# Optimization experiments

Hardware: AMD Instinct MI355X
Metric: run time of the kernel (lower is better)

## Reference

```python
import jax, jax.numpy as jnp
import numpy as np

N_NODES = 50000
N_EDGES = 1600000
IN_DIM = 128
HID = [128, 128]
OUT_DIM = 64
N_USERS = 10000


def setup_inputs() -> dict:
    key = jax.random.key(0)
    ks = jax.random.split(key, 12)
    features = jax.random.normal(ks[0], (N_NODES, IN_DIM), jnp.float32)
    src = jax.random.randint(ks[1], (N_EDGES,), 0, N_NODES)
    dst = jax.random.randint(ks[2], (N_EDGES,), 0, N_NODES)
    users = jax.random.randint(ks[3], (N_USERS,), 0, N_NODES)
    s = 0.05
    W0 = jax.random.normal(ks[4], (IN_DIM, HID[0]), jnp.float32) * s
    b0 = jnp.zeros((HID[0],), jnp.float32)
    W1 = jax.random.normal(ks[5], (HID[0], HID[1]), jnp.float32) * s
    b1 = jnp.zeros((HID[1],), jnp.float32)
    Ws1 = jax.random.normal(ks[6], (HID[1], 64), jnp.float32) * s
    bs1 = jnp.zeros((64,), jnp.float32)
    Ws2 = jax.random.normal(ks[7], (64, OUT_DIM), jnp.float32) * s
    bs2 = jnp.zeros((OUT_DIM,), jnp.float32)
    return {"features": features, "W0": W0, "b0": b0, "W1": W1, "b1": b1,
            "Ws1": Ws1, "bs1": bs1, "Ws2": Ws2, "bs2": bs2,
            "src": src, "dst": dst, "users": users}


def _gcn_layer(h, src, dst, cs, cd, W, b):
    # DGL GraphConv, norm='both': relu(D_in^-1/2 A D_out^-1/2 (h W) + b)
    h = h @ W                                   # [N, d_out]
    m = (h * cs)[src]                           # [E, d_out] gathered messages
    agg = jax.ops.segment_sum(m, dst, num_segments=N_NODES)
    return jax.nn.relu(agg * cd + b)


def reference(features, W0, b0, W1, b1, Ws1, bs1, Ws2, bs2, src, dst, users):
    ones = jnp.ones(src.shape[0], jnp.float32)
    deg_out = jax.ops.segment_sum(ones, src, num_segments=N_NODES)
    deg_in = jax.ops.segment_sum(ones, dst, num_segments=N_NODES)
    cs = jnp.maximum(deg_out, 1.0)[:, None] ** -0.5  # source-side norm
    cd = jnp.maximum(deg_in, 1.0)[:, None] ** -0.5   # dest-side norm
    h = _gcn_layer(features, src, dst, cs, cd, W0, b0)
    # dropout between layers: identity in eval mode
    h = _gcn_layer(h, src, dst, cs, cd, W1, b1)
    user_h = h[users]                            # [U, HID[-1]]
    R = jnp.tanh(user_h @ Ws1 + bs1) @ Ws2 + bs2  # SR head
    return (R, h)
```

## Files before the change

### kernel.cpp

```cpp
#include <hip/hip_runtime.h>
#include <hip/hip_bf16.h>
#include <hip/hip_fp16.h>

#define NN 50000
#define NE 1600000
#define DIM 128
#define NU 10000
#define NB 256
#define SLICE_W 12500
#define NE4 (NE / 4)
#define CHUNK4 ((NE4 + NB - 1) / NB)
#define NSC 49

__global__ __launch_bounds__(512) void k_hist(const int4* __restrict__ src4,
                                              const int4* __restrict__ dst4,
                                              unsigned int* __restrict__ histD,
                                              unsigned int* __restrict__ histS) {
    __shared__ unsigned int lh[SLICE_W];
    for (int i = threadIdx.x; i < SLICE_W; i += 512) lh[i] = 0u;
    __syncthreads();
    int b = blockIdx.x & (NB - 1);
    const int4* idx4 = (blockIdx.x < NB) ? dst4 : src4;
    unsigned int* out = ((blockIdx.x < NB) ? histD : histS) + (size_t)b * SLICE_W;
    int beg = b * CHUNK4, end = min(beg + CHUNK4, NE4);
    for (int i = beg + threadIdx.x; i < end; i += 512) {
        int4 v = idx4[i];
        atomicAdd(&lh[v.x >> 2], 1u << ((v.x & 3) * 8));
        atomicAdd(&lh[v.y >> 2], 1u << ((v.y & 3) * 8));
        atomicAdd(&lh[v.z >> 2], 1u << ((v.z & 3) * 8));
        atomicAdd(&lh[v.w >> 2], 1u << ((v.w & 3) * 8));
    }
    __syncthreads();
    for (int i = threadIdx.x; i < SLICE_W; i += 512) out[i] = lh[i];
}

__global__ __launch_bounds__(256) void k_reduce_norms(const unsigned int* __restrict__ histD,
                                                      const unsigned int* __restrict__ histS,
                                                      int* __restrict__ din,
                                                      float* __restrict__ cs, float* __restrict__ cd,
                                                      int* __restrict__ partials) {
    __shared__ int red[256];
    int wi = blockIdx.x * blockDim.x + threadIdx.x;
    unsigned int d0 = 0, d1 = 0, d2 = 0, d3 = 0, s0 = 0, s1 = 0, s2 = 0, s3 = 0;
    if (wi < SLICE_W) {
        for (int b = 0; b < NB; ++b) {
            unsigned int wd = histD[(size_t)b * SLICE_W + wi];
            unsigned int ws = histS[(size_t)b * SLICE_W + wi];
            d0 += wd & 0xFFu; d1 += (wd >> 8) & 0xFFu; d2 += (wd >> 16) & 0xFFu; d3 += wd >> 24;
            s0 += ws & 0xFFu; s1 += (ws >> 8) & 0xFFu; s2 += (ws >> 16) & 0xFFu; s3 += ws >> 24;
        }
        int n = wi * 4;
        *(int4*)&din[n] = make_int4(d0, d1, d2, d3);
        float4 vcd, vcs;
        vcd.x = rsqrtf(fmaxf((float)d0, 1.f)); vcd.y = rsqrtf(fmaxf((float)d1, 1.f));
        vcd.z = rsqrtf(fmaxf((float)d2, 1.f)); vcd.w = rsqrtf(fmaxf((float)d3, 1.f));
        vcs.x = rsqrtf(fmaxf((float)s0, 1.f)); vcs.y = rsqrtf(fmaxf((float)s1, 1.f));
        vcs.z = rsqrtf(fmaxf((float)s2, 1.f)); vcs.w = rsqrtf(fmaxf((float)s3, 1.f));
        *(float4*)&cd[n] = vcd;
        *(float4*)&cs[n] = vcs;
    }
    red[threadIdx.x] = (int)(d0 + d1 + d2 + d3);
    __syncthreads();
    for (int off = 128; off > 0; off >>= 1) {
        if (threadIdx.x < off) red[threadIdx.x] += red[threadIdx.x + off];
        __syncthreads();
    }
    if (threadIdx.x == 0) partials[blockIdx.x] = red[0];
}

__global__ __launch_bounds__(64) void k_scan2(const int* __restrict__ partials,
                                              int* __restrict__ bases) {
    int lane = threadIdx.x;
    int v = (lane < NSC) ? partials[lane] : 0;
    int s = v;
    for (int off = 1; off < 64; off <<= 1) {
        int n = __shfl_up(s, off);
        if (lane >= off) s += n;
    }
    if (lane < NSC) bases[lane] = s - v;
}

__global__ __launch_bounds__(256) void k_scan3(const int* __restrict__ din,
                                               const int* __restrict__ bases,
                                               int* __restrict__ offs) {
    __shared__ int part[256];
    int t = threadIdx.x;
    int n0 = blockIdx.x * 1024 + t * 4;
    int4 d = make_int4(0, 0, 0, 0);
    if (n0 < NN) d = *(const int4*)&din[n0];
    int tsum = d.x + d.y + d.z + d.w;
    part[t] = tsum;
    __syncthreads();
    for (int off = 1; off < 256; off <<= 1) {
        int v = (t >= off) ? part[t - off] : 0;
        __syncthreads();
        part[t] += v;
        __syncthreads();
    }
    if (n0 < NN) {
        int o = bases[blockIdx.x] + part[t] - tsum;
        *(int4*)&offs[n0] = make_int4(o, o + d.x, o + d.x + d.y, o + d.x + d.y + d.z);
    }
}

__global__ __launch_bounds__(256) void k_blockbase(const unsigned int* __restrict__ histD,
                                                   unsigned char* __restrict__ rel8) {
    int n = blockIdx.x * blockDim.x + threadIdx.x;
    if (n >= NN) return;
    int wi = n >> 2, sh = (n & 3) * 8;
    unsigned int run = 0;
    for (int b = 0; b < NB; ++b) {
        rel8[(size_t)b * NN + n] = (unsigned char)run;
        run += (histD[(size_t)b * SLICE_W + wi] >> sh) & 0xFFu;
    }
}

__global__ __launch_bounds__(512) void k_scatter2(const int4* __restrict__ src4,
                                                  const int4* __restrict__ dst4,
                                                  const int* __restrict__ offs,
                                                  const unsigned char* __restrict__ rel8,
                                                  unsigned short* __restrict__ csc) {
    __shared__ unsigned int lc[SLICE_W];
    for (int i = threadIdx.x; i < SLICE_W; i += 512) lc[i] = 0u;
    __syncthreads();
    int b = blockIdx.x;
    const unsigned char* rel = rel8 + (size_t)b * NN;
    int beg = b * CHUNK4, end = min(beg + CHUNK4, NE4);
    for (int i = beg + threadIdx.x; i < end; i += 512) {
        int4 s = src4[i];
        int4 d = dst4[i];
#pragma unroll
        for (int j = 0; j < 4; ++j) {
            int dd = (j == 0) ? d.x : (j == 1) ? d.y : (j == 2) ? d.z : d.w;
            int ss = (j == 0) ? s.x : (j == 1) ? s.y : (j == 2) ? s.z : s.w;
            int sh = (dd & 3) * 8;
            unsigned int old = atomicAdd(&lc[dd >> 2], 1u << sh);
            int local = (old >> sh) & 0xFF;
            csc[offs[dd] + rel[dd] + local] = (unsigned short)ss;
        }
    }
}

__global__ __launch_bounds__(256) void k_matmul_cs(const float* __restrict__ X,
                                                   const float* __restrict__ W,
                                                   const float* __restrict__ cs,
                                                   __half* __restrict__ Y, int nrows) {
    __shared__ __half sW[DIM * DIM];
    __shared__ float sX[16][DIM];
    for (int i = threadIdx.x * 4; i < DIM * DIM; i += 256 * 4) {
        float4 w4 = *(const float4*)&W[i];
        *(__half2*)&sW[i]     = __float22half2_rn(make_float2(w4.x, w4.y));
        *(__half2*)&sW[i + 2] = __float22half2_rn(make_float2(w4.z, w4.w));
    }
    int rl = threadIdx.x >> 6;
    int c = (threadIdx.x & 63) * 2;
    int ngroups = (nrows + 15) >> 4;
    for (int g = blockIdx.x; g < ngroups; g += gridDim.x) {
        __syncthreads();
        {
            int row = threadIdx.x >> 4;
            int col = (threadIdx.x & 15) * 8;
            int rr = min(g * 16 + row, nrows - 1);
            const float* xp = X + (size_t)rr * DIM + col;
            *(float4*)&sX[row][col] = *(const float4*)xp;
            *(float4*)&sX[row][col + 4] = *(const float4*)(xp + 4);
        }
        __syncthreads();
        float acc[4][2] = {};
#pragma unroll 4
        for (int k = 0; k < DIM; ++k) {
            float2 w = __half22float2(*(const __half2*)&sW[k * DIM + c]);
            float x0 = sX[rl * 4 + 0][k];
            float x1 = sX[rl * 4 + 1][k];
            float x2 = sX[rl * 4 + 2][k];
            float x3 = sX[rl * 4 + 3][k];
            acc[0][0] = fmaf(x0, w.x, acc[0][0]); acc[0][1] = fmaf(x0, w.y, acc[0][1]);
            acc[1][0] = fmaf(x1, w.x, acc[1][0]); acc[1][1] = fmaf(x1, w.y, acc[1][1]);
            acc[2][0] = fmaf(x2, w.x, acc[2][0]); acc[2][1] = fmaf(x2, w.y, acc[2][1]);
            acc[3][0] = fmaf(x3, w.x, acc[3][0]); acc[3][1] = fmaf(x3, w.y, acc[3][1]);
        }
#pragma unroll
        for (int j = 0; j < 4; ++j) {
            int r = g * 16 + rl * 4 + j;
            if (r < nrows) {
                float s = cs[r];
                __half2 hv = __float22half2_rn(make_float2(acc[j][0] * s, acc[j][1] * s));
                *(__half2*)&Y[(size_t)r * DIM + c] = hv;
            }
        }
    }
}

__global__ __launch_bounds__(256) void k_aggregate(const __half* __restrict__ hs,
                                                   const unsigned short* __restrict__ csc,
                                                   const int* __restrict__ offs,
                                                   const int* __restrict__ din,
                                                   const float* __restrict__ cd,
                                                   const float* __restrict__ bias,
                                                   float* __restrict__ out) {
    int wid = threadIdx.x >> 6;
    int lane = threadIdx.x & 63;
    int h = lane >> 5;
    int l = lane & 31;
    int d = blockIdx.x * 4 + wid;
    int beg = offs[d];
    int end = beg + din[d];
    const __half* base = hs + l * 4;
    float a0 = 0.f, a1 = 0.f, a2 = 0.f, a3 = 0.f;
    float b0 = 0.f, b1 = 0.f, b2 = 0.f, b3 = 0.f;
    float c0 = 0.f, c1 = 0.f, c2 = 0.f, c3 = 0.f;
    float e0 = 0.f, e1 = 0.f, e2 = 0.f, e3 = 0.f;
    int i = beg + h;
    for (; i + 14 < end; i += 16) {
        int sI[8];
#pragma unroll
        for (int j = 0; j < 8; ++j) sI[j] = csc[i + 2 * j];
        short4 vI[8];
#pragma unroll
        for (int j = 0; j < 8; ++j) vI[j] = *(const short4*)(base + (size_t)sI[j] * DIM);
#pragma unroll
        for (int j = 0; j < 8; j += 4) {
            float2 x0 = __half22float2(*(const __half2*)&vI[j].x);
            float2 x1 = __half22float2(*(const __half2*)&vI[j].z);
            float2 y0 = __half22float2(*(const __half2*)&vI[j + 1].x);
            float2 y1 = __half22float2(*(const __half2*)&vI[j + 1].z);
            float2 z0 = __half22float2(*(const __half2*)&vI[j + 2].x);
            float2 z1 = __half22float2(*(const __half2*)&vI[j + 2].z);
            float2 w0 = __half22float2(*(const __half2*)&vI[j + 3].x);
            float2 w1 = __half22float2(*(const __half2*)&vI[j + 3].z);
            a0 += x0.x; a1 += x0.y; a2 += x1.x; a3 += x1.y;
            b0 += y0.x; b1 += y0.y; b2 += y1.x; b3 += y1.y;
            c0 += z0.x; c1 += z0.y; c2 += z1.x; c3 += z1.y;
            e0 += w0.x; e1 += w0.y; e2 += w1.x; e3 += w1.y;
        }
    }
    for (; i + 6 < end; i += 8) {
        int s0 = csc[i], s1 = csc[i + 2], s2 = csc[i + 4], s3 = csc[i + 6];
        short4 v0 = *(const short4*)(base + (size_t)s0 * DIM);
        short4 v1 = *(const short4*)(base + (size_t)s1 * DIM);
        short4 v2 = *(const short4*)(base + (size_t)s2 * DIM);
        short4 v3 = *(const short4*)(base + (size_t)s3 * DIM);
        float2 x0 = __half22float2(*(const __half2*)&v0.x);
        float2 x1 = __half22float2(*(const __half2*)&v0.z);
        float2 y0 = __half22float2(*(const __half2*)&v1.x);
        float2 y1 = __half22float2(*(const __half2*)&v1.z);
        float2 z0 = __half22float2(*(const __half2*)&v2.x);
        float2 z1 = __half22float2(*(const __half2*)&v2.z);
        float2 w0 = __half22float2(*(const __half2*)&v3.x);
        float2 w1 = __half22float2(*(const __half2*)&v3.z);
        a0 += x0.x; a1 += x0.y; a2 += x1.x; a3 += x1.y;
        b0 += y0.x; b1 += y0.y; b2 += y1.x; b3 += y1.y;
        c0 += z0.x; c1 += z0.y; c2 += z1.x; c3 += z1.y;
        e0 += w0.x; e1 += w0.y; e2 += w1.x; e3 += w1.y;
    }
    for (; i < end; i += 2) {
        int s = csc[i];
        short4 v = *(const short4*)(base + (size_t)s * DIM);
        float2 x0 = __half22float2(*(const __half2*)&v.x);
        float2 x1 = __half22float2(*(const __half2*)&v.z);
        a0 += x0.x; a1 += x0.y; a2 += x1.x; a3 += x1.y;
    }
    a0 += b0 + c0 + e0; a1 += b1 + c1 + e1;
    a2 += b2 + c2 + e2; a3 += b3 + c3 + e3;
    a0 += __shfl(a0, lane ^ 32);
    a1 += __shfl(a1, lane ^ 32);
    a2 += __shfl(a2, lane ^ 32);
    a3 += __shfl(a3, lane ^ 32);
    if (h == 0) {
        float c = cd[d];
        float4 bv = *(const float4*)&bias[l * 4];
        float4 o;
        o.x = fmaxf(fmaf(a0, c, bv.x), 0.f);
        o.y = fmaxf(fmaf(a1, c, bv.y), 0.f);
        o.z = fmaxf(fmaf(a2, c, bv.z), 0.f);
        o.w = fmaxf(fmaf(a3, c, bv.w), 0.f);
        *(float4*)&out[(size_t)d * DIM + l * 4] = o;
    }
}

__global__ __launch_bounds__(256) void k_sr_head(const float* __restrict__ h,
                                                 const int* __restrict__ users,
                                                 const float* __restrict__ Ws1,
                                                 const float* __restrict__ bs1,
                                                 const float* __restrict__ Ws2,
                                                 const float* __restrict__ bs2,
                                                 float* __restrict__ R, int nu) {
    __shared__ float sW1[DIM * 64];
    __shared__ float sW2[64 * 64];
    __shared__ float sU[4][DIM];
    __shared__ float sT[4][64];
    for (int i = threadIdx.x * 4; i < DIM * 64; i += 256 * 4)
        *(float4*)&sW1[i] = *(const float4*)&Ws1[i];
    for (int i = threadIdx.x * 4; i < 64 * 64; i += 256 * 4)
        *(float4*)&sW2[i] = *(const float4*)&Ws2[i];
    int ul = threadIdx.x >> 6;
    int c = threadIdx.x & 63;
    for (int base = blockIdx.x * 4; base < nu; base += gridDim.x * 4) {
        int u = base + ul;
        __syncthreads();
        if (u < nu) {
            int node = users[u];
            *(float2*)&sU[ul][c * 2] = *(const float2*)&h[(size_t)node * DIM + c * 2];
        }
        __syncthreads();
        float t = 0.f;
        if (u < nu) {
            float acc = bs1[c];
#pragma unroll 8
            for (int k = 0; k < DIM; ++k) acc = fmaf(sU[ul][k], sW1[k * 64 + c], acc);
            t = tanhf(acc);
        }
        sT[ul][c] = t;
        __syncthreads();
        if (u < nu) {
            float acc = bs2[c];
#pragma unroll 8
            for (int k = 0; k < 64; ++k) acc = fmaf(sT[ul][k], sW2[k * 64 + c], acc);
            R[(size_t)u * 64 + c] = acc;
        }
    }
}

extern "C" void kernel_launch(void* const* d_in, const int* in_sizes, int n_in,
                              void* d_out, int out_size, void* d_ws, size_t ws_size,
                              hipStream_t stream) {
    const float* features = (const float*)d_in[0];
    const float* W0  = (const float*)d_in[1];
    const float* b0  = (const float*)d_in[2];
    const float* W1  = (const float*)d_in[3];
    const float* b1  = (const float*)d_in[4];
    const float* Ws1 = (const float*)d_in[5];
    const float* bs1 = (const float*)d_in[6];
    const float* Ws2 = (const float*)d_in[7];
    const float* bs2 = (const float*)d_in[8];
    const int* src   = (const int*)d_in[9];
    const int* dst   = (const int*)d_in[10];
    const int* users = (const int*)d_in[11];

    float* R = (float*)d_out;
    float* H = (float*)d_out + (size_t)NU * 64;

    char* ws = (char*)d_ws;
    __half* hsA  = (__half*)(ws + 0);
    unsigned int* histD = (unsigned int*)(ws + 0);
    unsigned int* histS = (unsigned int*)(ws + 12800000);
    unsigned char* rel8 = (unsigned char*)(ws + 12800000);
    unsigned short* csc = (unsigned short*)(ws + 25600000);
    int*   din   = (int*)  (ws + 28800000);
    float* cs    = (float*)(ws + 29000000);
    float* cd    = (float*)(ws + 29200000);
    int*   offs  = (int*)  (ws + 29400000);
    int*   partials = (int*)(ws + 29600000);
    int*   bases    = (int*)(ws + 29601024);

    k_hist<<<2 * NB, 512, 0, stream>>>((const int4*)src, (const int4*)dst, histD, histS);
    k_reduce_norms<<<NSC, 256, 0, stream>>>(histD, histS, din, cs, cd, partials);
    k_scan2<<<1, 64, 0, stream>>>(partials, bases);
    k_scan3<<<NSC, 256, 0, stream>>>(din, bases, offs);
    k_blockbase<<<(NN + 255) / 256, 256, 0, stream>>>(histD, rel8);
    k_scatter2<<<NB, 512, 0, stream>>>((const int4*)src, (const int4*)dst, offs, rel8, csc);

    k_matmul_cs<<<1024, 256, 0, stream>>>(features, W0, cs, hsA, NN);
    k_aggregate<<<12500, 256, 0, stream>>>(hsA, csc, offs, din, cd, b0, H);

    k_matmul_cs<<<1024, 256, 0, stream>>>(H, W1, cs, hsA, NN);
    k_aggregate<<<12500, 256, 0, stream>>>(hsA, csc, offs, din, cd, b1, H);

    k_sr_head<<<625, 256, 0, stream>>>(H, users, Ws1, bs1, Ws2, bs2, R, NU);
}
```

Measured before the change: 291.3 us.

## Split degree reduction across two thread groups and widen histogram/scatter blocks

The degree reduction kernel now uses 98 blocks with two 128-thread groups, each summing half of the 256 per-block histograms, then combining through shared memory. This doubles the parallelism of a latency-bound serial loop. The scan kernels are resized to match the new block count, with scan2 handling two partials per lane. The histogram and scatter kernels move from 512 to 1024 threads per block to raise occupancy on the edge loops, at the cost of fewer resident blocks per CU.

Result: faster. 285.2 us (-2.1%).

```diff
diff --git a/kernel.cpp b/kernel.cpp
--- a/kernel.cpp
+++ b/kernel.cpp
@@ -10,20 +10,20 @@
 #define SLICE_W 12500
 #define NE4 (NE / 4)
 #define CHUNK4 ((NE4 + NB - 1) / NB)
-#define NSC 49
-
-__global__ __launch_bounds__(512) void k_hist(const int4* __restrict__ src4,
-                                              const int4* __restrict__ dst4,
-                                              unsigned int* __restrict__ histD,
-                                              unsigned int* __restrict__ histS) {
+#define NRB 98
+
+__global__ __launch_bounds__(1024) void k_hist(const int4* __restrict__ src4,
+                                               const int4* __restrict__ dst4,
+                                               unsigned int* __restrict__ histD,
+                                               unsigned int* __restrict__ histS) {
     __shared__ unsigned int lh[SLICE_W];
-    for (int i = threadIdx.x; i < SLICE_W; i += 512) lh[i] = 0u;
+    for (int i = threadIdx.x; i < SLICE_W; i += 1024) lh[i] = 0u;
     __syncthreads();
     int b = blockIdx.x & (NB - 1);
     const int4* idx4 = (blockIdx.x < NB) ? dst4 : src4;
     unsigned int* out = ((blockIdx.x < NB) ? histD : histS) + (size_t)b * SLICE_W;
     int beg = b * CHUNK4, end = min(beg + CHUNK4, NE4);
-    for (int i = beg + threadIdx.x; i < end; i += 512) {
+    for (int i = beg + threadIdx.x; i < end; i += 1024) {
         int4 v = idx4[i];
         atomicAdd(&lh[v.x >> 2], 1u << ((v.x & 3) * 8));
         atomicAdd(&lh[v.y >> 2], 1u << ((v.y & 3) * 8));
@@ -31,7 +31,7 @@
         atomicAdd(&lh[v.w >> 2], 1u << ((v.w & 3) * 8));
     }
     __syncthreads();
-    for (int i = threadIdx.x; i < SLICE_W; i += 512) out[i] = lh[i];
+    for (int i = threadIdx.x; i < SLICE_W; i += 1024) out[i] = lh[i];
 }
 
 __global__ __launch_bounds__(256) void k_reduce_norms(const unsigned int* __restrict__ histD,
@@ -39,16 +39,29 @@
                                                       int* __restrict__ din,
                                                       float* __restrict__ cs, float* __restrict__ cd,
                                                       int* __restrict__ partials) {
+    __shared__ unsigned int part8[128][8];
     __shared__ int red[256];
-    int wi = blockIdx.x * blockDim.x + threadIdx.x;
+    int wl = threadIdx.x & 127;
+    int g = threadIdx.x >> 7;
+    int wi = blockIdx.x * 128 + wl;
     unsigned int d0 = 0, d1 = 0, d2 = 0, d3 = 0, s0 = 0, s1 = 0, s2 = 0, s3 = 0;
     if (wi < SLICE_W) {
-        for (int b = 0; b < NB; ++b) {
+        for (int b = g * 128; b < g * 128 + 128; ++b) {
             unsigned int wd = histD[(size_t)b * SLICE_W + wi];
             unsigned int ws = histS[(size_t)b * SLICE_W + wi];
             d0 += wd & 0xFFu; d1 += (wd >> 8) & 0xFFu; d2 += (wd >> 16) & 0xFFu; d3 += wd >> 24;
             s0 += ws & 0xFFu; s1 += (ws >> 8) & 0xFFu; s2 += (ws >> 16) & 0xFFu; s3 += ws >> 24;
         }
+    }
+    red[threadIdx.x] = (int)(d0 + d1 + d2 + d3);
+    if (g == 1) {
+        part8[wl][0] = d0; part8[wl][1] = d1; part8[wl][2] = d2; part8[wl][3] = d3;
+        part8[wl][4] = s0; part8[wl][5] = s1; part8[wl][6] = s2; part8[wl][7] = s3;
+    }
+    __syncthreads();
+    if (g == 0 && wi < SLICE_W) {
+        d0 += part8[wl][0]; d1 += part8[wl][1]; d2 += part8[wl][2]; d3 += part8[wl][3];
+        s0 += part8[wl][4]; s1 += part8[wl][5]; s2 += part8[wl][6]; s3 += part8[wl][7];
         int n = wi * 4;
         *(int4*)&din[n] = make_int4(d0, d1, d2, d3);
         float4 vcd, vcs;
@@ -59,8 +72,6 @@
         *(float4*)&cd[n] = vcd;
         *(float4*)&cs[n] = vcs;
     }
-    red[threadIdx.x] = (int)(d0 + d1 + d2 + d3);
-    __syncthreads();
     for (int off = 128; off > 0; off >>= 1) {
         if (threadIdx.x < off) red[threadIdx.x] += red[threadIdx.x + off];
         __syncthreads();
@@ -71,27 +82,31 @@
 __global__ __launch_bounds__(64) void k_scan2(const int* __restrict__ partials,
                                               int* __restrict__ bases) {
     int lane = threadIdx.x;
-    int v = (lane < NSC) ? partials[lane] : 0;
-    int s = v;
+    int p0 = (2 * lane < NRB) ? partials[2 * lane] : 0;
+    int p1 = (2 * lane + 1 < NRB) ? partials[2 * lane + 1] : 0;
+    int pair = p0 + p1;
+    int s = pair;
     for (int off = 1; off < 64; off <<= 1) {
         int n = __shfl_up(s, off);
         if (lane >= off) s += n;
     }
-    if (lane < NSC) bases[lane] = s - v;
-}
-
-__global__ __launch_bounds__(256) void k_scan3(const int* __restrict__ din,
+    int excl = s - pair;
+    if (2 * lane < NRB) bases[2 * lane] = excl;
+    if (2 * lane + 1 < NRB) bases[2 * lane + 1] = excl + p0;
+}
+
+__global__ __launch_bounds__(128) void k_scan3(const int* __restrict__ din,
                                                const int* __restrict__ bases,
                                                int* __restrict__ offs) {
-    __shared__ int part[256];
+    __shared__ int part[128];
     int t = threadIdx.x;
-    int n0 = blockIdx.x * 1024 + t * 4;
+    int n0 = blockIdx.x * 512 + t * 4;
     int4 d = make_int4(0, 0, 0, 0);
     if (n0 < NN) d = *(const int4*)&din[n0];
     int tsum = d.x + d.y + d.z + d.w;
     part[t] = tsum;
     __syncthreads();
-    for (int off = 1; off < 256; off <<= 1) {
+    for (int off = 1; off < 128; off <<= 1) {
         int v = (t >= off) ? part[t - off] : 0;
         __syncthreads();
         part[t] += v;
@@ -115,18 +130,18 @@
     }
 }
 
-__global__ __launch_bounds__(512) void k_scatter2(const int4* __restrict__ src4,
-                                                  const int4* __restrict__ dst4,
-                                                  const int* __restrict__ offs,
-                                                  const unsigned char* __restrict__ rel8,
-                                                  unsigned short* __restrict__ csc) {
+__global__ __launch_bounds__(1024) void k_scatter2(const int4* __restrict__ src4,
+                                                   const int4* __restrict__ dst4,
+                                                   const int* __restrict__ offs,
+                                                   const unsigned char* __restrict__ rel8,
+                                                   unsigned short* __restrict__ csc) {
     __shared__ unsigned int lc[SLICE_W];
-    for (int i = threadIdx.x; i < SLICE_W; i += 512) lc[i] = 0u;
+    for (int i = threadIdx.x; i < SLICE_W; i += 1024) lc[i] = 0u;
     __syncthreads();
     int b = blockIdx.x;
     const unsigned char* rel = rel8 + (size_t)b * NN;
     int beg = b * CHUNK4, end = min(beg + CHUNK4, NE4);
-    for (int i = beg + threadIdx.x; i < end; i += 512) {
+    for (int i = beg + threadIdx.x; i < end; i += 1024) {
         int4 s = src4[i];
         int4 d = dst4[i];
 #pragma unroll
@@ -353,12 +368,12 @@
     int*   partials = (int*)(ws + 29600000);
     int*   bases    = (int*)(ws + 29601024);
 
-    k_hist<<<2 * NB, 512, 0, stream>>>((const int4*)src, (const int4*)dst, histD, histS);
-    k_reduce_norms<<<NSC, 256, 0, stream>>>(histD, histS, din, cs, cd, partials);
+    k_hist<<<2 * NB, 1024, 0, stream>>>((const int4*)src, (const int4*)dst, histD, histS);
+    k_reduce_norms<<<NRB, 256, 0, stream>>>(histD, histS, din, cs, cd, partials);
     k_scan2<<<1, 64, 0, stream>>>(partials, bases);
-    k_scan3<<<NSC, 256, 0, stream>>>(din, bases, offs);
+    k_scan3<<<NRB, 128, 0, stream>>>(din, bases, offs);
     k_blockbase<<<(NN + 255) / 256, 256, 0, stream>>>(histD, rel8);
-    k_scatter2<<<NB, 512, 0, stream>>>((const int4*)src, (const int4*)dst, offs, rel8, csc);
+    k_scatter2<<<NB, 1024, 0, stream>>>((const int4*)src, (const int4*)dst, offs, rel8, csc);
 
     k_matmul_cs<<<1024, 256, 0, stream>>>(features, W0, cs, hsA, NN);
     k_aggregate<<<12500, 256, 0, stream>>>(hsA, csc, offs, din, cd, b0, H);
```
